# Kernel optimization log

Hardware: AMD Instinct MI355X
Metric: run time of the kernel (lower is better)

Reference implementation:

```python
import jax, jax.numpy as jnp
import numpy as np

B, N, C = 2, 2048, 768
H = 12
HD = C // H  # 64
EPS = 1e-6


def setup_inputs() -> dict:
    key = jax.random.key(0)
    ks = jax.random.split(key, 6)
    x = jax.random.normal(ks[0], (B, N, C), dtype=jnp.float32)
    # Xavier-uniform-ish init for kernels
    lim_qkv = float(np.sqrt(6.0 / (C + 3 * C)))
    lim_proj = float(np.sqrt(6.0 / (C + C)))
    qkv_kernel = jax.random.uniform(ks[1], (C, 3 * C), minval=-lim_qkv, maxval=lim_qkv, dtype=jnp.float32)
    qkv_bias = jnp.zeros((3 * C,), dtype=jnp.float32)
    proj_kernel = jax.random.uniform(ks[2], (C, C), minval=-lim_proj, maxval=lim_proj, dtype=jnp.float32)
    proj_bias = jnp.zeros((C,), dtype=jnp.float32)
    q_norm_w = jnp.ones((HD,), dtype=jnp.float32)
    k_norm_w = jnp.ones((HD,), dtype=jnp.float32)
    # Standard RoPE tables: freqs over half the head dim, tiled to full head_dim
    half = HD // 2
    inv_freq = 1.0 / (10000.0 ** (jnp.arange(0, half, dtype=jnp.float32) / half))
    t = jnp.arange(N, dtype=jnp.float32)
    freqs = jnp.outer(t, inv_freq)               # (N, HD/2)
    emb = jnp.concatenate([freqs, freqs], axis=-1)  # (N, HD)
    rope_cos = jnp.cos(emb)
    rope_sin = jnp.sin(emb)
    return {"x": x, "rope_cos": rope_cos, "rope_sin": rope_sin,
            "qkv_kernel": qkv_kernel, "qkv_bias": qkv_bias,
            "proj_kernel": proj_kernel, "proj_bias": proj_bias,
            "q_norm_w": q_norm_w, "k_norm_w": k_norm_w}


def _rms_norm(x, w):
    var = jnp.mean(x * x, axis=-1, keepdims=True)
    return x * jax.lax.rsqrt(var + EPS) * w


def _rope(x, cos, sin):
    # x: (B, H, N, HD); cos/sin: (N, HD)
    half = x.shape[-1] // 2
    x1, x2 = x[..., :half], x[..., half:]
    rot = jnp.concatenate([-x2, x1], axis=-1)
    return x * cos + rot * sin


def reference(x, rope_cos, rope_sin, qkv_kernel, qkv_bias, proj_kernel, proj_bias, q_norm_w, k_norm_w):
    b, n, c = x.shape
    qkv = x @ qkv_kernel + qkv_bias                       # (B, N, 3C)
    qkv = qkv.reshape(b, n, 3, H, HD).transpose(2, 0, 3, 1, 4)  # (3, B, H, N, HD)
    q, k, v = qkv[0], qkv[1], qkv[2]
    q = _rope(_rms_norm(q, q_norm_w), rope_cos, rope_sin)
    k = _rope(_rms_norm(k, k_norm_w), rope_cos, rope_sin)
    scale = 1.0 / jnp.sqrt(jnp.float32(HD)).astype(x.dtype)
    attn = jnp.einsum('bhqd,bhkd->bhqk', q, k) * scale    # (B, H, N, N)
    attn = jax.nn.softmax(attn, axis=-1)
    out = jnp.einsum('bhqk,bhkd->bhqd', attn, v)          # (B, H, N, HD)
    out = out.swapaxes(1, 2).reshape(b, n, c)
    return out @ proj_kernel + proj_bias
```

## Files before the change

### kernel.cpp

```cpp
#include <hip/hip_runtime.h>
#include <math.h>

#define B_    2
#define N_    2048
#define C_    768
#define H_    12
#define HD_   64
#define NROWS (B_*N_)
#define QKVC  (3*C_)
#define EPSV  1e-6f
#define SCALE 0.125f
#define LOG2E 1.44269504088896f
#define SMAX  12.0f

typedef unsigned short u16;
typedef short bf16x8 __attribute__((ext_vector_type(8)));
typedef float f32x4  __attribute__((ext_vector_type(4)));

__device__ __forceinline__ float b2f(u16 u) {
    unsigned v = ((unsigned)u) << 16;
    return __builtin_bit_cast(float, v);
}
__device__ __forceinline__ u16 f2b(float f) {
    unsigned u = __builtin_bit_cast(unsigned, f);
    u += 0x7fffu + ((u >> 16) & 1u);
    return (u16)(u >> 16);
}
__device__ __forceinline__ unsigned pk2(float a, float b) {
#if __has_builtin(__builtin_amdgcn_cvt_pk_bf16_f32)
    auto r = __builtin_amdgcn_cvt_pk_bf16_f32(a, b);
    return __builtin_bit_cast(unsigned, r);
#else
    return (unsigned)f2b(a) | ((unsigned)f2b(b) << 16);
#endif
}
__device__ __forceinline__ float fexp2(float x) {
#if __has_builtin(__builtin_amdgcn_exp2f)
    return __builtin_amdgcn_exp2f(x);
#else
    return exp2f(x);
#endif
}
__device__ __forceinline__ void gload_lds16(const void* g, void* l) {
    __builtin_amdgcn_global_load_lds(
        (const __attribute__((address_space(1))) unsigned int*)g,
        (__attribute__((address_space(3))) unsigned int*)l, 16, 0, 0);
}

__global__ __launch_bounds__(256)
void cvt_bf16_kernel(const float* __restrict__ src, u16* __restrict__ dst) {
    const int i = (blockIdx.x * 256 + threadIdx.x) * 4;
    const float4 v = *(const float4*)(src + i);
    uint2 o = { pk2(v.x, v.y), pk2(v.z, v.w) };
    *(uint2*)(dst + i) = o;
}

__global__ __launch_bounds__(256)
void wtrans_kernel(const float* __restrict__ W, u16* __restrict__ Wt,
                   int K, int N) {
    __shared__ float T[64][65];
    const int k0 = blockIdx.y * 64, n0 = blockIdx.x * 64;
    const int t = threadIdx.x, r = t >> 6, c = t & 63;
#pragma unroll
    for (int p = 0; p < 16; ++p) {
        const int kl = p * 4 + r;
        T[kl][c] = W[(size_t)(k0 + kl) * N + n0 + c];
    }
    __syncthreads();
#pragma unroll
    for (int p = 0; p < 16; ++p) {
        const int nl = p * 4 + r;
        Wt[(size_t)(n0 + nl) * K + k0 + c] = f2b(T[c][nl]);
    }
}

template <bool BF16OUT>
__global__ __launch_bounds__(256)
void gemm_tn_kernel(const u16* __restrict__ A, const u16* __restrict__ Bt,
                    const float* __restrict__ bias, void* __restrict__ Cout,
                    int M, int N, int K) {
    __shared__ __attribute__((aligned(16))) u16 As[128 * 32];
    __shared__ __attribute__((aligned(16))) u16 Bs[128 * 32];
    const int tid = threadIdx.x;
    const int w = tid >> 6, l = tid & 63;
    const int lq = l & 15, quad = l >> 4;
    const int mbase = blockIdx.y * 128, nbase = blockIdx.x * 128;

    f32x4 acc[4][4];
    const f32x4 z4 = {0.f, 0.f, 0.f, 0.f};
#pragma unroll
    for (int mb = 0; mb < 4; ++mb)
#pragma unroll
        for (int nb = 0; nb < 4; ++nb) acc[mb][nb] = z4;

    const int srow = (l >> 2);
    const int sdc  = (l & 3) ^ ((l >> 2) & 3);

    for (int k0 = 0; k0 < K; k0 += 32) {
#pragma unroll
        for (int cc = 0; cc < 2; ++cc) {
            const int c = 2 * w + cc;
            const int row = 16 * c + srow;
            gload_lds16(A  + (size_t)(mbase + row) * K + k0 + sdc * 8, &As[c * 512]);
            gload_lds16(Bt + (size_t)(nbase + row) * K + k0 + sdc * 8, &Bs[c * 512]);
        }
        __syncthreads();

        bf16x8 af[4], bfr[4];
#pragma unroll
        for (int mb = 0; mb < 4; ++mb)
            af[mb] = *(const bf16x8*)
                &As[((w >> 1) * 64 + mb * 16 + lq) * 32 + ((quad ^ (lq & 3)) * 8)];
#pragma unroll
        for (int nb = 0; nb < 4; ++nb)
            bfr[nb] = *(const bf16x8*)
                &Bs[((w & 1) * 64 + nb * 16 + lq) * 32 + ((quad ^ (lq & 3)) * 8)];
#pragma unroll
        for (int mb = 0; mb < 4; ++mb)
#pragma unroll
            for (int nb = 0; nb < 4; ++nb)
                acc[mb][nb] = __builtin_amdgcn_mfma_f32_16x16x32_bf16(
                    af[mb], bfr[nb], acc[mb][nb], 0, 0, 0);
        __syncthreads();
    }

#pragma unroll
    for (int nb = 0; nb < 4; ++nb) {
        const int col = nbase + (w & 1) * 64 + nb * 16 + lq;
        const float bv = bias[col];
#pragma unroll
        for (int mb = 0; mb < 4; ++mb) {
#pragma unroll
            for (int r = 0; r < 4; ++r) {
                const int row = mbase + (w >> 1) * 64 + mb * 16 + quad * 4 + r;
                const float v = acc[mb][nb][r] + bv;
                if (BF16OUT) ((u16*)Cout)[(size_t)row * N + col] = f2b(v);
                else         ((float*)Cout)[(size_t)row * N + col] = v;
            }
        }
    }
}

__global__ __launch_bounds__(256)
void normrope_kernel(u16* __restrict__ qkv, u16* __restrict__ kpack,
                     const float* __restrict__ cosb,
                     const float* __restrict__ sinb,
                     const float* __restrict__ qw,
                     const float* __restrict__ kw) {
    const int item = blockIdx.x * 16 + (threadIdx.x >> 4);
    const int lq   = threadIdx.x & 15;
    const int h    = item % H_;
    const int row  = item / H_;
    const int n    = row & (N_ - 1);
    const int b    = row >> 11;
    const size_t base = (size_t)row * QKVC + h * HD_ + lq * 4;

    const ushort4 q4 = *(const ushort4*)&qkv[base];
    const ushort4 k4 = *(const ushort4*)&qkv[base + C_];
    float qf[4], kf[4];
    qf[0] = b2f(q4.x); qf[1] = b2f(q4.y); qf[2] = b2f(q4.z); qf[3] = b2f(q4.w);
    kf[0] = b2f(k4.x); kf[1] = b2f(k4.y); kf[2] = b2f(k4.z); kf[3] = b2f(k4.w);

    float q2 = qf[0]*qf[0] + qf[1]*qf[1] + qf[2]*qf[2] + qf[3]*qf[3];
    float k2 = kf[0]*kf[0] + kf[1]*kf[1] + kf[2]*kf[2] + kf[3]*kf[3];
#pragma unroll
    for (int off = 8; off >= 1; off >>= 1) {
        q2 += __shfl_xor(q2, off, 64);
        k2 += __shfl_xor(k2, off, 64);
    }
    const float rq = rsqrtf(q2 * (1.f / 64.f) + EPSV);
    const float rk = rsqrtf(k2 * (1.f / 64.f) + EPSV);

    const float4 qwv = *(const float4*)&qw[lq * 4];
    const float4 kwv = *(const float4*)&kw[lq * 4];
    const float4 cv  = *(const float4*)&cosb[n * HD_ + lq * 4];
    const float4 sv  = *(const float4*)&sinb[n * HD_ + lq * 4];

    float qn[4], kn[4];
    qn[0] = qf[0]*rq*qwv.x; qn[1] = qf[1]*rq*qwv.y;
    qn[2] = qf[2]*rq*qwv.z; qn[3] = qf[3]*rq*qwv.w;
    kn[0] = kf[0]*rk*kwv.x; kn[1] = kf[1]*rk*kwv.y;
    kn[2] = kf[2]*rk*kwv.z; kn[3] = kf[3]*rk*kwv.w;

    const float sgn = (lq < 8) ? -1.f : 1.f;
    float qo[4], ko[4];
    const float cc[4] = {cv.x, cv.y, cv.z, cv.w};
    const float ss[4] = {sv.x, sv.y, sv.z, sv.w};
#pragma unroll
    for (int j = 0; j < 4; ++j) {
        const float qp = __shfl_xor(qn[j], 8, 64);
        const float kp = __shfl_xor(kn[j], 8, 64);
        qo[j] = (qn[j] * cc[j] + sgn * qp * ss[j]) * (SCALE * LOG2E);
        ko[j] =  kn[j] * cc[j] + sgn * kp * ss[j];
    }
    uint2 qout = { pk2(qo[0], qo[1]), pk2(qo[2], qo[3]) };
    uint2 kout = { pk2(ko[0], ko[1]), pk2(ko[2], ko[3]) };
    *(uint2*)&qkv[base] = qout;

    const int kt = n >> 6, kr = n & 63;
    const int kb = kr >> 4, m = kr & 15;
    const int ks = lq >> 3, quad = (lq >> 1) & 3, jj = (lq & 1) * 4;
    const size_t off = ((size_t)(b * H_ + h) * 32 + kt) * 4096
                     + (size_t)((kb * 2 + ks) * 64 + quad * 16 + m) * 8 + jj;
    *(uint2*)&kpack[off] = kout;
}

__global__ __launch_bounds__(256)
void vpack_kernel(const u16* __restrict__ qkv, u16* __restrict__ vpack) {
    __shared__ u16 Tv[64][72];
    const int kt = blockIdx.x, bh = blockIdx.y;
    const int b = bh / H_, h = bh % H_;
    const int t = threadIdx.x;
    {
        const int r = t >> 2, seg = t & 3;
        const u16* src = &qkv[(size_t)(b * N_ + kt * 64 + r) * QKVC
                              + 2 * C_ + h * HD_ + seg * 16];
        const uint4 v0 = *(const uint4*)src;
        const uint4 v1 = *(const uint4*)(src + 8);
        *(uint4*)&Tv[r][seg * 16]     = v0;
        *(uint4*)&Tv[r][seg * 16 + 8] = v1;
    }
    __syncthreads();
    u16 tmp[16];
#pragma unroll
    for (int g2 = 0; g2 < 2; ++g2) {
        const int g = t * 2 + g2;
        const int mbks = g >> 6;
        const int l  = g & 63;
        const int mb = mbks >> 1, ks = mbks & 1;
        const int m  = l & 15,  quad = l >> 4;
#pragma unroll
        for (int j = 0; j < 8; ++j)
            tmp[g2 * 8 + j] = Tv[ks * 32 + quad * 8 + j][mb * 16 + m];
    }
    u16* dst = &vpack[((size_t)bh * 32 + kt) * 4096 + t * 16];
    *(uint4*)dst       = *(const uint4*)&tmp[0];
    *(uint4*)(dst + 8) = *(const uint4*)&tmp[8];
}

#define NQ_   2
#define QB_   (NQ_ * 16)
#define NQT_  (N_ / QB_)

__global__ __launch_bounds__(128, 3)
void flash_mfma_kernel(const u16* __restrict__ qkv,
                       const u16* __restrict__ kpack,
                       const u16* __restrict__ vpack,
                       u16* __restrict__ attnb) {
    __shared__ __attribute__((aligned(16))) u16 Ps[2][QB_ * 64];
    __shared__ __attribute__((aligned(16))) float Oex[QB_ * 64];
    __shared__ float lex[QB_];

    const int tid = threadIdx.x;
    const int w = tid >> 6, l = tid & 63;
    const int lq = l & 15, quad = l >> 4;
    const int sw = lq & 7;

    const int lin  = blockIdx.x;
    const int slot = lin >> 3;
    const int bh   = (lin & 7) * 3 + (slot / NQT_);
    const int qt   = slot & (NQT_ - 1);
    const int b = bh / H_, h = bh % H_;
    const size_t qbase = (size_t)b * N_ * QKVC + h * HD_;
    const size_t tbase = (size_t)bh * 32 * 4096;

    bf16x8 qb[NQ_][2];
#pragma unroll
    for (int nq = 0; nq < NQ_; ++nq)
#pragma unroll
        for (int ks = 0; ks < 2; ++ks)
            qb[nq][ks] = *(const bf16x8*)
                &qkv[qbase + (size_t)(qt * QB_ + nq * 16 + lq) * QKVC
                     + ks * 32 + quad * 8];

    float lsum[NQ_];
#pragma unroll
    for (int nq = 0; nq < NQ_; ++nq) lsum[nq] = 0.f;
    f32x4 oacc[4][NQ_];
    const f32x4 z4 = {0.f, 0.f, 0.f, 0.f};
#pragma unroll
    for (int mb = 0; mb < 4; ++mb)
#pragma unroll
        for (int nq = 0; nq < NQ_; ++nq) oacc[mb][nq] = z4;

    bf16x8 ka[4][2];
#pragma unroll
    for (int kb = 0; kb < 4; ++kb)
#pragma unroll
        for (int ks = 0; ks < 2; ++ks)
            ka[kb][ks] = *(const bf16x8*)
                &kpack[tbase + (size_t)w * 4096 + ((kb * 2 + ks) * 64 + l) * 8];

    for (int kt2 = 0; kt2 < 16; ++kt2) {
        const int kt  = 2 * kt2 + w;
        const int ktn = (kt + 2) & 31;
        const size_t vb = tbase + (size_t)kt * 4096;
        const size_t kb_n = tbase + (size_t)ktn * 4096;

        bf16x8 va[4][2];
#pragma unroll
        for (int mb = 0; mb < 4; ++mb)
#pragma unroll
            for (int ks = 0; ks < 2; ++ks)
                va[mb][ks] = *(const bf16x8*)
                    &vpack[vb + ((mb * 2 + ks) * 64 + l) * 8];

#pragma unroll
        for (int kb = 0; kb < 4; ++kb) {
            f32x4 sacc[NQ_];
#pragma unroll
            for (int nq = 0; nq < NQ_; ++nq) sacc[nq] = z4;
#pragma unroll
            for (int ks = 0; ks < 2; ++ks)
#pragma unroll
                for (int nq = 0; nq < NQ_; ++nq)
                    sacc[nq] = __builtin_amdgcn_mfma_f32_16x16x32_bf16(
                        ka[kb][ks], qb[nq][ks], sacc[nq], 0, 0, 0);
#pragma unroll
            for (int nq = 0; nq < NQ_; ++nq) {
                float p[4];
#pragma unroll
                for (int r = 0; r < 4; ++r) p[r] = fexp2(sacc[nq][r] - SMAX);
                lsum[nq] += (p[0] + p[1]) + (p[2] + p[3]);
                uint2 pkv = { pk2(p[0], p[1]), pk2(p[2], p[3]) };
                *(uint2*)&Ps[w][(nq * 16 + lq) * 64
                                + (((kb * 2 + (quad >> 1)) ^ sw) * 8)
                                + (quad & 1) * 4] = pkv;
            }
        }

#pragma unroll
        for (int kb = 0; kb < 4; ++kb)
#pragma unroll
            for (int ks = 0; ks < 2; ++ks)
                ka[kb][ks] = *(const bf16x8*)
                    &kpack[kb_n + ((kb * 2 + ks) * 64 + l) * 8];

        bf16x8 pb[2][NQ_];
#pragma unroll
        for (int ks = 0; ks < 2; ++ks)
#pragma unroll
            for (int nq = 0; nq < NQ_; ++nq)
                pb[ks][nq] = *(const bf16x8*)
                    &Ps[w][(nq * 16 + lq) * 64 + (((ks * 4 + quad) ^ sw) * 8)];

#pragma unroll
        for (int mb = 0; mb < 4; ++mb)
#pragma unroll
            for (int ks = 0; ks < 2; ++ks)
#pragma unroll
                for (int nq = 0; nq < NQ_; ++nq)
                    oacc[mb][nq] = __builtin_amdgcn_mfma_f32_16x16x32_bf16(
                        va[mb][ks], pb[ks][nq], oacc[mb][nq], 0, 0, 0);
    }

#pragma unroll
    for (int nq = 0; nq < NQ_; ++nq) {
        lsum[nq] += __shfl_xor(lsum[nq], 16, 64);
        lsum[nq] += __shfl_xor(lsum[nq], 32, 64);
    }

    if (w == 1) {
#pragma unroll
        for (int nq = 0; nq < NQ_; ++nq) {
#pragma unroll
            for (int mb = 0; mb < 4; ++mb) {
                const int chunk = (mb * 4 + quad) ^ lq;
                *(float4*)&Oex[(nq * 16 + lq) * 64 + chunk * 4] =
                    *(float4*)&oacc[mb][nq];
            }
            if (quad == 0) lex[nq * 16 + lq] = lsum[nq];
        }
    }
    __syncthreads();
    if (w == 0) {
#pragma unroll
        for (int nq = 0; nq < NQ_; ++nq) {
            const int qrow = nq * 16 + lq;
            const float inv = 1.f / (lsum[nq] + lex[qrow]);
#pragma unroll
            for (int mb = 0; mb < 4; ++mb) {
                const int chunk = (mb * 4 + quad) ^ lq;
                const float4 oe = *(const float4*)&Oex[qrow * 64 + chunk * 4];
                const float o0 = (oacc[mb][nq][0] + oe.x) * inv;
                const float o1 = (oacc[mb][nq][1] + oe.y) * inv;
                const float o2 = (oacc[mb][nq][2] + oe.z) * inv;
                const float o3 = (oacc[mb][nq][3] + oe.w) * inv;
                uint2 ov = { pk2(o0, o1), pk2(o2, o3) };
                *(uint2*)&Ps[0][qrow * 64
                                + (((mb * 2 + (quad >> 1)) ^ sw) * 8)
                                + (quad & 1) * 4] = ov;
            }
        }
#pragma unroll
        for (int pass = 0; pass < QB_ / 8; ++pass) {
            const int ql = pass * 8 + (l >> 3);
            const int c  = l & 7;
            const bf16x8 v = *(const bf16x8*)&Ps[0][ql * 64 + ((c ^ (ql & 7)) * 8)];
            const int query = qt * QB_ + ql;
            *(bf16x8*)&attnb[(size_t)(b * N_ + query) * C_ + h * HD_ + c * 8] = v;
        }
    }
}

extern "C" void kernel_launch(void* const* d_in, const int* in_sizes, int n_in,
                              void* d_out, int out_size, void* d_ws, size_t ws_size,
                              hipStream_t stream) {
    const float* x        = (const float*)d_in[0];
    const float* rope_cos = (const float*)d_in[1];
    const float* rope_sin = (const float*)d_in[2];
    const float* qkv_w    = (const float*)d_in[3];
    const float* qkv_b    = (const float*)d_in[4];
    const float* proj_w   = (const float*)d_in[5];
    const float* proj_b   = (const float*)d_in[6];
    const float* q_nw     = (const float*)d_in[7];
    const float* k_nw     = (const float*)d_in[8];
    float* out = (float*)d_out;

    u16* xb    = (u16*)d_ws;
    u16* qwt   = xb    + (size_t)NROWS * C_;
    u16* pwt   = qwt   + (size_t)QKVC * C_;
    u16* qkvb  = pwt   + (size_t)C_ * C_;
    u16* vpackb= qkvb  + (size_t)NROWS * QKVC;
    u16* attnb = vpackb+ (size_t)B_ * H_ * 32 * 4096;
    u16* kpackb= xb;

    cvt_bf16_kernel<<<dim3(NROWS * C_ / 1024), 256, 0, stream>>>(x, xb);
    wtrans_kernel<<<dim3(QKVC / 64, C_ / 64), 256, 0, stream>>>(qkv_w, qwt, C_, QKVC);
    wtrans_kernel<<<dim3(C_ / 64, C_ / 64), 256, 0, stream>>>(proj_w, pwt, C_, C_);

    gemm_tn_kernel<true><<<dim3(QKVC / 128, NROWS / 128), 256, 0, stream>>>(
        xb, qwt, qkv_b, qkvb, NROWS, QKVC, C_);

    normrope_kernel<<<dim3(NROWS * H_ / 16), 256, 0, stream>>>(
        qkvb, kpackb, rope_cos, rope_sin, q_nw, k_nw);

    vpack_kernel<<<dim3(32, B_ * H_), 256, 0, stream>>>(qkvb, vpackb);

    flash_mfma_kernel<<<dim3(B_ * H_ * NQT_), 128, 0, stream>>>(
        qkvb, kpackb, vpackb, attnb);

    gemm_tn_kernel<false><<<dim3(C_ / 128, NROWS / 128), 256, 0, stream>>>(
        attnb, pwt, proj_b, out, NROWS, C_, C_);
}
```

Before: 195.0 us.

## Narrow output-projection GEMM tile, remap GEMM blocks across XCDs, prioritise MFMA waves

The GEMM kernel gets a templated N-tile width, and the output projection uses 64-wide tiles so it launches twice as many workgroups for its small 768-column output. Block indices are remapped so consecutive tiles land on the same XCD, which should improve L2 reuse. In the flash attention kernel, s_setprio raises wave priority around the MFMA blocks so matrix work is issued ahead of the exp/store work of other waves. The narrower tile lowers the arithmetic intensity per block, and the remap assumes the workgroup count divides evenly by 8.

Measured after the change: 180.4 us. -7.5%, faster.

```diff
diff --git a/kernel.cpp b/kernel.cpp
--- a/kernel.cpp
+++ b/kernel.cpp
@@ -74,24 +74,30 @@
     }
 }
 
-template <bool BF16OUT>
+template <bool BF16OUT, int BN>
 __global__ __launch_bounds__(256)
 void gemm_tn_kernel(const u16* __restrict__ A, const u16* __restrict__ Bt,
                     const float* __restrict__ bias, void* __restrict__ Cout,
                     int M, int N, int K) {
+    constexpr int NB = BN / 32;
     __shared__ __attribute__((aligned(16))) u16 As[128 * 32];
-    __shared__ __attribute__((aligned(16))) u16 Bs[128 * 32];
+    __shared__ __attribute__((aligned(16))) u16 Bs[BN * 32];
     const int tid = threadIdx.x;
     const int w = tid >> 6, l = tid & 63;
     const int lq = l & 15, quad = l >> 4;
-    const int mbase = blockIdx.y * 128, nbase = blockIdx.x * 128;
-
-    f32x4 acc[4][4];
+
+    const int gx  = gridDim.x;
+    const int nwg = gx * gridDim.y;
+    const int d   = blockIdx.x + gx * blockIdx.y;
+    const int lin = (d & 7) * (nwg >> 3) + (d >> 3);
+    const int mbase = (lin / gx) * 128, nbase = (lin % gx) * BN;
+
+    f32x4 acc[4][NB];
     const f32x4 z4 = {0.f, 0.f, 0.f, 0.f};
 #pragma unroll
     for (int mb = 0; mb < 4; ++mb)
 #pragma unroll
-        for (int nb = 0; nb < 4; ++nb) acc[mb][nb] = z4;
+        for (int nb = 0; nb < NB; ++nb) acc[mb][nb] = z4;
 
     const int srow = (l >> 2);
     const int sdc  = (l & 3) ^ ((l >> 2) & 3);
@@ -101,32 +107,37 @@
         for (int cc = 0; cc < 2; ++cc) {
             const int c = 2 * w + cc;
             const int row = 16 * c + srow;
-            gload_lds16(A  + (size_t)(mbase + row) * K + k0 + sdc * 8, &As[c * 512]);
+            gload_lds16(A + (size_t)(mbase + row) * K + k0 + sdc * 8, &As[c * 512]);
+        }
+#pragma unroll
+        for (int cc = 0; cc < BN / 64; ++cc) {
+            const int c = (BN / 64) * w + cc;
+            const int row = 16 * c + srow;
             gload_lds16(Bt + (size_t)(nbase + row) * K + k0 + sdc * 8, &Bs[c * 512]);
         }
         __syncthreads();
 
-        bf16x8 af[4], bfr[4];
+        bf16x8 af[4], bfr[NB];
 #pragma unroll
         for (int mb = 0; mb < 4; ++mb)
             af[mb] = *(const bf16x8*)
                 &As[((w >> 1) * 64 + mb * 16 + lq) * 32 + ((quad ^ (lq & 3)) * 8)];
 #pragma unroll
-        for (int nb = 0; nb < 4; ++nb)
+        for (int nb = 0; nb < NB; ++nb)
             bfr[nb] = *(const bf16x8*)
-                &Bs[((w & 1) * 64 + nb * 16 + lq) * 32 + ((quad ^ (lq & 3)) * 8)];
+                &Bs[((w & 1) * (BN / 2) + nb * 16 + lq) * 32 + ((quad ^ (lq & 3)) * 8)];
 #pragma unroll
         for (int mb = 0; mb < 4; ++mb)
 #pragma unroll
-            for (int nb = 0; nb < 4; ++nb)
+            for (int nb = 0; nb < NB; ++nb)
                 acc[mb][nb] = __builtin_amdgcn_mfma_f32_16x16x32_bf16(
                     af[mb], bfr[nb], acc[mb][nb], 0, 0, 0);
         __syncthreads();
     }
 
 #pragma unroll
-    for (int nb = 0; nb < 4; ++nb) {
-        const int col = nbase + (w & 1) * 64 + nb * 16 + lq;
+    for (int nb = 0; nb < NB; ++nb) {
+        const int col = nbase + (w & 1) * (BN / 2) + nb * 16 + lq;
         const float bv = bias[col];
 #pragma unroll
         for (int mb = 0; mb < 4; ++mb) {
@@ -310,12 +321,14 @@
             f32x4 sacc[NQ_];
 #pragma unroll
             for (int nq = 0; nq < NQ_; ++nq) sacc[nq] = z4;
+            __builtin_amdgcn_s_setprio(1);
 #pragma unroll
             for (int ks = 0; ks < 2; ++ks)
 #pragma unroll
                 for (int nq = 0; nq < NQ_; ++nq)
                     sacc[nq] = __builtin_amdgcn_mfma_f32_16x16x32_bf16(
                         ka[kb][ks], qb[nq][ks], sacc[nq], 0, 0, 0);
+            __builtin_amdgcn_s_setprio(0);
 #pragma unroll
             for (int nq = 0; nq < NQ_; ++nq) {
                 float p[4];
@@ -344,6 +357,7 @@
                 pb[ks][nq] = *(const bf16x8*)
                     &Ps[w][(nq * 16 + lq) * 64 + (((ks * 4 + quad) ^ sw) * 8)];
 
+        __builtin_amdgcn_s_setprio(1);
 #pragma unroll
         for (int mb = 0; mb < 4; ++mb)
 #pragma unroll
@@ -352,6 +366,7 @@
                 for (int nq = 0; nq < NQ_; ++nq)
                     oacc[mb][nq] = __builtin_amdgcn_mfma_f32_16x16x32_bf16(
                         va[mb][ks], pb[ks][nq], oacc[mb][nq], 0, 0, 0);
+        __builtin_amdgcn_s_setprio(0);
     }
 
 #pragma unroll
@@ -429,7 +444,7 @@
     wtrans_kernel<<<dim3(QKVC / 64, C_ / 64), 256, 0, stream>>>(qkv_w, qwt, C_, QKVC);
     wtrans_kernel<<<dim3(C_ / 64, C_ / 64), 256, 0, stream>>>(proj_w, pwt, C_, C_);
 
-    gemm_tn_kernel<true><<<dim3(QKVC / 128, NROWS / 128), 256, 0, stream>>>(
+    gemm_tn_kernel<true, 128><<<dim3(QKVC / 128, NROWS / 128), 256, 0, stream>>>(
         xb, qwt, qkv_b, qkvb, NROWS, QKVC, C_);
 
     normrope_kernel<<<dim3(NROWS * H_ / 16), 256, 0, stream>>>(
@@ -440,6 +455,6 @@
     flash_mfma_kernel<<<dim3(B_ * H_ * NQT_), 128, 0, stream>>>(
         qkvb, kpackb, vpackb, attnb);
 
-    gemm_tn_kernel<false><<<dim3(C_ / 128, NROWS / 128), 256, 0, stream>>>(
+    gemm_tn_kernel<false, 64><<<dim3(C_ / 64, NROWS / 128), 256, 0, stream>>>(
         attnb, pwt, proj_b, out, NROWS, C_, C_);
 }
```
